# Performance work log

Measured on AMD Instinct MI355X. Metric: run time of the kernel, lower is better.

The kernel has to match this reference:

```python
import jax, jax.numpy as jnp
import numpy as np

NEG_INF = -1e30

def masked_softmax(logits, mask, axis):
    # mask broadcastable to logits; 1 = keep, 0 = mask out
    masked = jnp.where(mask > 0, logits, NEG_INF)
    return jax.nn.softmax(masked, axis=axis)

def setup_inputs() -> dict:
    key = jax.random.key(0)
    ks = jax.random.split(key, 6)
    B, H, C, Q = 64, 128, 1024, 128
    c = jax.random.normal(ks[0], (B, H, C), dtype=jnp.float32)
    q = jax.random.normal(ks[1], (B, H, Q), dtype=jnp.float32)
    c_mask = jnp.ones((B, C), dtype=jnp.float32)
    q_mask = jnp.ones((B, Q), dtype=jnp.float32)
    # xavier_uniform for (H,1): bound = sqrt(6/(H+1))
    bnd_v = float(np.sqrt(6.0 / (H + 1)))
    context_weights = jax.random.uniform(ks[2], (H, 1), minval=-bnd_v, maxval=bnd_v, dtype=jnp.float32)
    query_weights = jax.random.uniform(ks[3], (H, 1), minval=-bnd_v, maxval=bnd_v, dtype=jnp.float32)
    # xavier_uniform for (1,1,H): fan_in=1, fan_out=H -> bound = sqrt(6/(1+H))
    cq_weights = jax.random.uniform(ks[4], (1, 1, H), minval=-bnd_v, maxval=bnd_v, dtype=jnp.float32)
    bias = jnp.zeros((1,), dtype=jnp.float32)
    return {"c": c, "q": q, "c_mask": c_mask, "q_mask": q_mask,
            "context_weights": context_weights, "query_weights": query_weights,
            "cq_weights": cq_weights, "bias": bias}

def reference(c, q, c_mask, q_mask, context_weights, query_weights, cq_weights, bias):
    # to (B, len, H)
    c = jnp.swapaxes(c, 1, 2)  # (B, c_len, H)
    q = jnp.swapaxes(q, 1, 2)  # (B, q_len, H)
    B, c_len, H = c.shape
    q_len = q.shape[1]
    # trilinear similarity: (B, c_len, q_len)
    s0 = c @ context_weights                         # (B, c_len, 1)
    s1 = jnp.swapaxes(q @ query_weights, 1, 2)       # (B, 1, q_len)
    s2 = jnp.einsum('bch,bqh->bcq', c * cq_weights, q)
    S = s0 + s1 + s2 + bias
    a_att = masked_softmax(S, q_mask[:, None, :], axis=2)  # softmax over q_len
    b_att = masked_softmax(S, c_mask[:, :, None], axis=1)  # softmax over c_len
    a = jnp.einsum('bcq,bqh->bch', a_att, q)
    b = jnp.einsum('bcq,bkq,bkh->bch', a_att, b_att, c)
    x = jnp.concatenate([c, a, c * a, c * b], axis=2)  # (B, c_len, 4H)
    return jnp.swapaxes(x, 1, 2)  # (B, 4H, c_len)
```

## Files before the change

kernel.cpp:

```cpp
#include <hip/hip_runtime.h>
#include <math.h>

#define NEG_HUGE -1e30f
constexpr int B_ = 64, H_ = 128, C_ = 1024, Q_ = 128;

typedef __bf16 bf16x8 __attribute__((ext_vector_type(8)));
typedef float f32x4 __attribute__((ext_vector_type(4)));
typedef short short8 __attribute__((ext_vector_type(8)));
typedef short short4s __attribute__((ext_vector_type(4)));

__device__ __forceinline__ float bs2f(short s) {
  unsigned u = ((unsigned)(unsigned short)s) << 16;
  float f; __builtin_memcpy(&f, &u, 4); return f;
}
__device__ __forceinline__ short f2bs(float f) {
  unsigned u; __builtin_memcpy(&u, &f, 4);
  u = (u + 0x7fffu + ((u >> 16) & 1u)) >> 16;
  return (short)u;
}

__global__ __launch_bounds__(256) void kTc(const float* __restrict__ cin,
                                           const float* __restrict__ ctxw,
                                           short* __restrict__ cT,
                                           float* __restrict__ s0p) {
  __shared__ float T[64 * 69];
  const int t = threadIdx.x;
  const int c0 = blockIdx.x * 64, h0 = blockIdx.y * 64, b = blockIdx.z;
  {
    const int row = t >> 2, off = t & 3;
    const float* src = cin + (b * H_ + h0 + row) * C_ + c0;
#pragma unroll
    for (int j = 0; j < 4; ++j) {
      float4 v = *(const float4*)&src[off * 16 + j * 4];
      int cbase = off * 16 + j * 4;
      T[row * 69 + cbase + 0] = v.x;
      T[row * 69 + cbase + 1] = v.y;
      T[row * 69 + cbase + 2] = v.z;
      T[row * 69 + cbase + 3] = v.w;
    }
  }
  __syncthreads();
  {
    const int c = t >> 2, offh = t & 3;
    short* dst = cT + (b * C_ + c0 + c) * H_ + h0;
#pragma unroll
    for (int j = 0; j < 4; ++j) {
      int hs = offh * 16 + j * 4;
      short4s v;
      v[0] = f2bs(T[(hs + 0) * 69 + c]);
      v[1] = f2bs(T[(hs + 1) * 69 + c]);
      v[2] = f2bs(T[(hs + 2) * 69 + c]);
      v[3] = f2bs(T[(hs + 3) * 69 + c]);
      *(short4s*)&dst[hs] = v;
    }
  }
  if (t < 64) {
    float acc = 0.f;
#pragma unroll 8
    for (int h = 0; h < 64; ++h) acc += T[h * 69 + t] * ctxw[h0 + h];
    s0p[blockIdx.y * (B_ * C_) + b * C_ + c0 + t] = acc;
  }
}

__global__ __launch_bounds__(256) void kq(const float* __restrict__ qin,
                                          const float* __restrict__ qw,
                                          const float* __restrict__ cqw,
                                          const float* __restrict__ qmask,
                                          short* __restrict__ qTw,
                                          short* __restrict__ qbf,
                                          float* __restrict__ s1m) {
  __shared__ float T[64 * 130];
  const int t = threadIdx.x;
  const int q0 = blockIdx.x * 64, b = blockIdx.y;
#pragma unroll
  for (int p = 0; p < 8; ++p) {
    int fidx = t + 256 * p;
    int h = fidx >> 4, seg = fidx & 15;
    float4 v = *(const float4*)&qin[(b * H_ + h) * Q_ + q0 + seg * 4];
    T[(seg * 4 + 0) * 130 + h] = v.x;
    T[(seg * 4 + 1) * 130 + h] = v.y;
    T[(seg * 4 + 2) * 130 + h] = v.z;
    T[(seg * 4 + 3) * 130 + h] = v.w;
    short4s o; o[0] = f2bs(v.x); o[1] = f2bs(v.y); o[2] = f2bs(v.z); o[3] = f2bs(v.w);
    *(short4s*)&qbf[(b * H_ + h) * Q_ + q0 + seg * 4] = o;
  }
  __syncthreads();
  if (t < 64) {
    float acc = 0.f;
#pragma unroll 8
    for (int h = 0; h < 128; ++h) acc += T[t * 130 + h] * qw[h];
    float qm = (qmask[b * Q_ + q0 + t] > 0.f) ? 0.f : NEG_HUGE;
    s1m[b * Q_ + q0 + t] = acc + qm;
  }
  {
    const int q = t >> 2, off = t & 3;
    short* dst = qTw + (b * Q_ + q0 + q) * H_;
#pragma unroll
    for (int j = 0; j < 4; ++j) {
      int hbv = off * 32 + j * 8;
      short8 v;
#pragma unroll
      for (int i = 0; i < 8; ++i) v[i] = f2bs(T[q * 130 + hbv + i] * cqw[hbv + i]);
      *(short8*)&dst[hbv] = v;
    }
  }
}

__global__ __launch_bounds__(256) void k1_mfma(
    const short* __restrict__ cT, const short* __restrict__ qTw,
    const float* __restrict__ s1m, const float* __restrict__ cmask,
    const float* __restrict__ s0p,
    short* __restrict__ a_att, short* __restrict__ ePT,
    float* __restrict__ pcm, float* __restrict__ pcs) {
  __shared__ __align__(16) char uni[34816];
  __shared__ float s1mL[128], scolL[128], pw[512], mpL[128];
  short* AL = (short*)uni;
  short* BL = (short*)(uni + 10240);
  short* RP = (short*)uni;

  const int t = threadIdx.x;
  const int w = t >> 6, l = t & 63, quad = l >> 4, lcol = l & 15;
  const int bx = blockIdx.x, b = blockIdx.y, c0 = bx * 128;

  if (t < 128) {
    s1mL[t] = s1m[b * Q_ + t];
    float cm = (cmask[b * C_ + c0 + t] > 0.f) ? 0.f : NEG_HUGE;
    scolL[t] = cm + s0p[b * C_ + c0 + t] + s0p[B_ * C_ + b * C_ + c0 + t];
  }

  f32x4 acc[2][8];
#pragma unroll
  for (int mt = 0; mt < 2; ++mt)
#pragma unroll
    for (int nt = 0; nt < 8; ++nt) acc[mt][nt] = (f32x4){0.f, 0.f, 0.f, 0.f};

  const int ar = t >> 2, aoff = t & 3;

  for (int kc = 0; kc < 4; ++kc) {
    const int h0 = kc * 32;
    *(short8*)&AL[ar * 40 + aoff * 8] =
        *(const short8*)&cT[(b * C_ + c0 + ar) * H_ + h0 + aoff * 8];
    *(short8*)&AL[(64 + ar) * 40 + aoff * 8] =
        *(const short8*)&cT[(b * C_ + c0 + 64 + ar) * H_ + h0 + aoff * 8];
    *(short8*)&BL[ar * 40 + aoff * 8] =
        *(const short8*)&qTw[(b * Q_ + ar) * H_ + h0 + aoff * 8];
    *(short8*)&BL[(64 + ar) * 40 + aoff * 8] =
        *(const short8*)&qTw[(b * Q_ + 64 + ar) * H_ + h0 + aoff * 8];
    __syncthreads();
    bf16x8 af0 = *(bf16x8*)&AL[(w * 32 + lcol) * 40 + quad * 8];
    bf16x8 af1 = *(bf16x8*)&AL[(w * 32 + 16 + lcol) * 40 + quad * 8];
#pragma unroll
    for (int nt = 0; nt < 8; ++nt) {
      bf16x8 bfrag = *(bf16x8*)&BL[(nt * 16 + lcol) * 40 + quad * 8];
      acc[0][nt] = __builtin_amdgcn_mfma_f32_16x16x32_bf16(af0, bfrag, acc[0][nt], 0, 0, 0);
      acc[1][nt] = __builtin_amdgcn_mfma_f32_16x16x32_bf16(af1, bfrag, acc[1][nt], 0, 0, 0);
    }
    __syncthreads();
  }

  float s1v[8];
#pragma unroll
  for (int nt = 0; nt < 8; ++nt) s1v[nt] = s1mL[nt * 16 + lcol];
  float rm[2][4], inv[2][4];
#pragma unroll
  for (int mt = 0; mt < 2; ++mt)
#pragma unroll
    for (int r = 0; r < 4; ++r) {
      float m = -INFINITY;
#pragma unroll
      for (int nt = 0; nt < 8; ++nt) m = fmaxf(m, acc[mt][nt][r] + s1v[nt]);
      rm[mt][r] = m;
    }
#pragma unroll
  for (int d = 1; d <= 8; d <<= 1)
#pragma unroll
    for (int mt = 0; mt < 2; ++mt)
#pragma unroll
      for (int r = 0; r < 4; ++r)
        rm[mt][r] = fmaxf(rm[mt][r], __shfl_xor(rm[mt][r], d));
#pragma unroll
  for (int mt = 0; mt < 2; ++mt)
#pragma unroll
    for (int r = 0; r < 4; ++r) {
      float s = 0.f;
#pragma unroll
      for (int nt = 0; nt < 8; ++nt)
        s += __expf(acc[mt][nt][r] + s1v[nt] - rm[mt][r]);
      inv[mt][r] = s;
    }
#pragma unroll
  for (int d = 1; d <= 8; d <<= 1)
#pragma unroll
    for (int mt = 0; mt < 2; ++mt)
#pragma unroll
      for (int r = 0; r < 4; ++r)
        inv[mt][r] += __shfl_xor(inv[mt][r], d);
#pragma unroll
  for (int mt = 0; mt < 2; ++mt)
#pragma unroll
    for (int r = 0; r < 4; ++r) inv[mt][r] = 1.f / inv[mt][r];

#pragma unroll
  for (int mt = 0; mt < 2; ++mt)
#pragma unroll
    for (int nt = 0; nt < 8; ++nt)
#pragma unroll
      for (int r = 0; r < 4; ++r) {
        int row = w * 32 + mt * 16 + quad * 4 + r;
        int col = nt * 16 + lcol;
        float v = __expf(acc[mt][nt][r] + s1v[nt] - rm[mt][r]) * inv[mt][r];
        RP[row * 136 + col] = f2bs(v);
      }
  __syncthreads();
  {
    const int row = t >> 1, half = t & 1;
    short* dst = a_att + (b * C_ + c0 + row) * Q_ + half * 64;
    const short* srcp = RP + row * 136 + half * 64;
#pragma unroll
    for (int j = 0; j < 8; ++j) *(short8*)&dst[j * 8] = *(const short8*)&srcp[j * 8];
  }

  float cs0[2][4];
#pragma unroll
  for (int mt = 0; mt < 2; ++mt)
#pragma unroll
    for (int r = 0; r < 4; ++r)
      cs0[mt][r] = scolL[w * 32 + mt * 16 + quad * 4 + r];
  float pmv[8];
#pragma unroll
  for (int nt = 0; nt < 8; ++nt) {
    float m = -INFINITY;
#pragma unroll
    for (int mt = 0; mt < 2; ++mt)
#pragma unroll
      for (int r = 0; r < 4; ++r) m = fmaxf(m, acc[mt][nt][r] + cs0[mt][r]);
    pmv[nt] = m;
  }
#pragma unroll
  for (int nt = 0; nt < 8; ++nt) {
    pmv[nt] = fmaxf(pmv[nt], __shfl_xor(pmv[nt], 16));
    pmv[nt] = fmaxf(pmv[nt], __shfl_xor(pmv[nt], 32));
  }
  if (l < 16) {
#pragma unroll
    for (int nt = 0; nt < 8; ++nt) pw[w * 128 + nt * 16 + lcol] = pmv[nt];
  }
  __syncthreads();
  if (t < 128) {
    float m = fmaxf(fmaxf(pw[t], pw[128 + t]), fmaxf(pw[256 + t], pw[384 + t]));
    mpL[t] = m;
    pcm[(b * 8 + bx) * Q_ + t] = m;
  }
  __syncthreads();
  float mpv[8];
#pragma unroll
  for (int nt = 0; nt < 8; ++nt) mpv[nt] = mpL[nt * 16 + lcol];
  float psv[8];
#pragma unroll
  for (int nt = 0; nt < 8; ++nt) {
    float s = 0.f;
#pragma unroll
    for (int mt = 0; mt < 2; ++mt)
#pragma unroll
      for (int r = 0; r < 4; ++r)
        s += __expf(acc[mt][nt][r] + cs0[mt][r] - mpv[nt]);
    psv[nt] = s;
  }
#pragma unroll
  for (int nt = 0; nt < 8; ++nt) {
    psv[nt] += __shfl_xor(psv[nt], 16);
    psv[nt] += __shfl_xor(psv[nt], 32);
  }
  if (l < 16) {
#pragma unroll
    for (int nt = 0; nt < 8; ++nt) pw[w * 128 + nt * 16 + lcol] = psv[nt];
  }
  __syncthreads();
  if (t < 128) pcs[(b * 8 + bx) * Q_ + t] = pw[t] + pw[128 + t] + pw[256 + t] + pw[384 + t];

#pragma unroll
  for (int mt = 0; mt < 2; ++mt)
#pragma unroll
    for (int nt = 0; nt < 8; ++nt)
#pragma unroll
      for (int r = 0; r < 4; ++r) {
        int qq = nt * 16 + lcol;
        int cl = w * 32 + mt * 16 + quad * 4 + r;
        float v = __expf(acc[mt][nt][r] + cs0[mt][r] - mpv[nt]);
        RP[qq * 136 + cl] = f2bs(v);
      }
  __syncthreads();
  {
    const int qq = t >> 1, half = t & 1;
    short* dst = ePT + (b * Q_ + qq) * C_ + c0 + half * 64;
    const short* srcp = RP + qq * 136 + half * 64;
#pragma unroll
    for (int j = 0; j < 8; ++j) *(short8*)&dst[j * 8] = *(const short8*)&srcp[j * 8];
  }
}

__global__ __launch_bounds__(128) void k2b(const float* __restrict__ pcm,
                                           const float* __restrict__ pcs,
                                           float* __restrict__ scale_t,
                                           float* __restrict__ inv_cs) {
  const int b = blockIdx.x, q = threadIdx.x;
  float m[8]; float M = -INFINITY;
#pragma unroll
  for (int k = 0; k < 8; ++k) { m[k] = pcm[(b * 8 + k) * Q_ + q]; M = fmaxf(M, m[k]); }
  float s = 0.f;
#pragma unroll
  for (int k = 0; k < 8; ++k) {
    float sc = __expf(m[k] - M);
    scale_t[(b * 8 + k) * Q_ + q] = sc;
    s += pcs[(b * 8 + k) * Q_ + q] * sc;
  }
  inv_cs[b * Q_ + q] = 1.f / s;
}

__global__ __launch_bounds__(256) void krs(short* __restrict__ ePT,
                                           const float* __restrict__ scale_t) {
  const int gid = blockIdx.x * 256 + threadIdx.x;
  const int e = gid * 8;
  const int c = e & 1023, q = (e >> 10) & 127, b = e >> 17;
  const float s = scale_t[(b * 8 + (c >> 7)) * Q_ + q];
  short8 v = *(short8*)&ePT[e];
  short8 o;
#pragma unroll
  for (int i = 0; i < 8; ++i) o[i] = f2bs(bs2f(v[i]) * s);
  *(short8*)&ePT[e] = o;
}

__global__ __launch_bounds__(256) void k3_T(
    const short* __restrict__ ePs, const float* __restrict__ cin,
    float* __restrict__ Tpart) {
  __shared__ __align__(16) char uni[34816];
  short* AL = (short*)uni;
  short* BL = (short*)(uni + 10240);
  float* RPF = (float*)uni;
  const int t = threadIdx.x;
  const int w = t >> 6, l = t & 63, quad = l >> 4, lcol = l & 15;
  const int hb = blockIdx.x * 64, kc = blockIdx.y, b = blockIdx.z;

  f32x4 acc[2][4];
#pragma unroll
  for (int mt = 0; mt < 2; ++mt)
#pragma unroll
    for (int nt = 0; nt < 4; ++nt) acc[mt][nt] = (f32x4){0.f, 0.f, 0.f, 0.f};

  const int ar = t >> 2, aoff = t & 3;
  for (int ck = 0; ck < 8; ++ck) {
    const int coff = kc * 256 + ck * 32;
    *(short8*)&AL[ar * 40 + aoff * 8] =
        *(const short8*)&ePs[(b * Q_ + ar) * C_ + coff + aoff * 8];
    *(short8*)&AL[(64 + ar) * 40 + aoff * 8] =
        *(const short8*)&ePs[(b * Q_ + 64 + ar) * C_ + coff + aoff * 8];
    {
      const float* srcp = cin + (b * H_ + hb + ar) * C_ + coff + aoff * 8;
      short8 o;
#pragma unroll
      for (int i = 0; i < 8; ++i) o[i] = f2bs(srcp[i]);
      *(short8*)&BL[ar * 40 + aoff * 8] = o;
    }
    __syncthreads();
    bf16x8 af0 = *(bf16x8*)&AL[(w * 32 + lcol) * 40 + quad * 8];
    bf16x8 af1 = *(bf16x8*)&AL[(w * 32 + 16 + lcol) * 40 + quad * 8];
#pragma unroll
    for (int nt = 0; nt < 4; ++nt) {
      bf16x8 bfrag = *(bf16x8*)&BL[(nt * 16 + lcol) * 40 + quad * 8];
      acc[0][nt] = __builtin_amdgcn_mfma_f32_16x16x32_bf16(af0, bfrag, acc[0][nt], 0, 0, 0);
      acc[1][nt] = __builtin_amdgcn_mfma_f32_16x16x32_bf16(af1, bfrag, acc[1][nt], 0, 0, 0);
    }
    __syncthreads();
  }
#pragma unroll
  for (int mt = 0; mt < 2; ++mt)
#pragma unroll
    for (int nt = 0; nt < 4; ++nt)
#pragma unroll
      for (int r = 0; r < 4; ++r)
        RPF[(nt * 16 + lcol) * 136 + (w * 32 + mt * 16 + quad * 4 + r)] = acc[mt][nt][r];
  __syncthreads();
  {
    float* Tp = Tpart + (size_t)kc * (B_ * H_ * Q_) + ((size_t)b * H_ + hb) * Q_;
    const int lr = t >> 5, coln = (t & 31) * 4;
#pragma unroll
    for (int iter = 0; iter < 8; ++iter) {
      int hl = iter * 8 + lr;
      *(float4*)&Tp[hl * Q_ + coln] = *(float4*)&RPF[hl * 136 + coln];
    }
  }
}

__global__ __launch_bounds__(256) void k3b(const float* __restrict__ Tpart,
                                           const float* __restrict__ inv_cs,
                                           short* __restrict__ TmT) {
  const int gid = blockIdx.x * 256 + threadIdx.x;
  const int e = gid * 4;
  const int q0 = e & 127, b = e >> 14;
  float4 s = make_float4(0.f, 0.f, 0.f, 0.f);
#pragma unroll
  for (int k = 0; k < 4; ++k) {
    float4 v = *(const float4*)&Tpart[(size_t)k * (B_ * H_ * Q_) + e];
    s.x += v.x; s.y += v.y; s.z += v.z; s.w += v.w;
  }
  float4 ic = *(const float4*)&inv_cs[b * Q_ + q0];
  short4s o;
  o[0] = f2bs(s.x * ic.x); o[1] = f2bs(s.y * ic.y);
  o[2] = f2bs(s.z * ic.z); o[3] = f2bs(s.w * ic.w);
  *(short4s*)&TmT[e] = o;
}

__global__ __launch_bounds__(256) void k4_out(
    const short* __restrict__ a_att, const short* __restrict__ qbf,
    const short* __restrict__ TmT, const float* __restrict__ cin,
    float* __restrict__ out) {
  __shared__ __align__(16) char uni[34816];
  short* AL = (short*)uni;
  short* B1 = (short*)(uni + 10240);
  short* B2 = (short*)(uni + 15360);
  float* RPF = (float*)uni;
  const int t = threadIdx.x;
  const int w = t >> 6, l = t & 63, quad = l >> 4, lcol = l & 15;
  const int c0 = blockIdx.x * 128, hb = blockIdx.y * 64, b = blockIdx.z;

  f32x4 accA[2][4], accB[2][4];
#pragma unroll
  for (int mt = 0; mt < 2; ++mt)
#pragma unroll
    for (int nt = 0; nt < 4; ++nt) {
      accA[mt][nt] = (f32x4){0.f, 0.f, 0.f, 0.f};
      accB[mt][nt] = (f32x4){0.f, 0.f, 0.f, 0.f};
    }

  const int ar = t >> 2, aoff = t & 3;
  for (int kc = 0; kc < 4; ++kc) {
    const int q0 = kc * 32;
    *(short8*)&AL[ar * 40 + aoff * 8] =
        *(const short8*)&a_att[(b * C_ + c0 + ar) * Q_ + q0 + aoff * 8];
    *(short8*)&AL[(64 + ar) * 40 + aoff * 8] =
        *(const short8*)&a_att[(b * C_ + c0 + 64 + ar) * Q_ + q0 + aoff * 8];
    *(short8*)&B1[ar * 40 + aoff * 8] =
        *(const short8*)&qbf[(b * H_ + hb + ar) * Q_ + q0 + aoff * 8];
    *(short8*)&B2[ar * 40 + aoff * 8] =
        *(const short8*)&TmT[(b * H_ + hb + ar) * Q_ + q0 + aoff * 8];
    __syncthreads();
    bf16x8 af0 = *(bf16x8*)&AL[(w * 32 + lcol) * 40 + quad * 8];
    bf16x8 af1 = *(bf16x8*)&AL[(w * 32 + 16 + lcol) * 40 + quad * 8];
#pragma unroll
    for (int nt = 0; nt < 4; ++nt) {
      bf16x8 bq = *(bf16x8*)&B1[(nt * 16 + lcol) * 40 + quad * 8];
      bf16x8 bt = *(bf16x8*)&B2[(nt * 16 + lcol) * 40 + quad * 8];
      accA[0][nt] = __builtin_amdgcn_mfma_f32_16x16x32_bf16(af0, bq, accA[0][nt], 0, 0, 0);
      accA[1][nt] = __builtin_amdgcn_mfma_f32_16x16x32_bf16(af1, bq, accA[1][nt], 0, 0, 0);
      accB[0][nt] = __builtin_amdgcn_mfma_f32_16x16x32_bf16(af0, bt, accB[0][nt], 0, 0, 0);
      accB[1][nt] = __builtin_amdgcn_mfma_f32_16x16x32_bf16(af1, bt, accB[1][nt], 0, 0, 0);
    }
    __syncthreads();
  }

  const int lr = t >> 5, coln = (t & 31) * 4;
  float* ob = out + (size_t)b * 512 * 1024;
  float4 cvv[8];

#pragma unroll
  for (int mt = 0; mt < 2; ++mt)
#pragma unroll
    for (int nt = 0; nt < 4; ++nt)
#pragma unroll
      for (int r = 0; r < 4; ++r)
        RPF[(nt * 16 + lcol) * 136 + (w * 32 + mt * 16 + quad * 4 + r)] = accA[mt][nt][r];
  __syncthreads();
#pragma unroll
  for (int iter = 0; iter < 8; ++iter) {
    int hl = iter * 8 + lr;
    int hrow = hb + hl;
    float4 la = *(float4*)&RPF[hl * 136 + coln];
    float4 cv = *(const float4*)&cin[(b * H_ + hrow) * C_ + c0 + coln];
    cvv[iter] = cv;
    *(float4*)&ob[(size_t)hrow * 1024 + c0 + coln] = cv;
    *(float4*)&ob[(size_t)(128 + hrow) * 1024 + c0 + coln] = la;
    float4 p = make_float4(cv.x * la.x, cv.y * la.y, cv.z * la.z, cv.w * la.w);
    *(float4*)&ob[(size_t)(256 + hrow) * 1024 + c0 + coln] = p;
  }
  __syncthreads();
#pragma unroll
  for (int mt = 0; mt < 2; ++mt)
#pragma unroll
    for (int nt = 0; nt < 4; ++nt)
#pragma unroll
      for (int r = 0; r < 4; ++r)
        RPF[(nt * 16 + lcol) * 136 + (w * 32 + mt * 16 + quad * 4 + r)] = accB[mt][nt][r];
  __syncthreads();
#pragma unroll
  for (int iter = 0; iter < 8; ++iter) {
    int hl = iter * 8 + lr;
    int hrow = hb + hl;
    float4 lb = *(float4*)&RPF[hl * 136 + coln];
    float4 cv = cvv[iter];
    float4 p = make_float4(cv.x * lb.x, cv.y * lb.y, cv.z * lb.z, cv.w * lb.w);
    *(float4*)&ob[(size_t)(384 + hrow) * 1024 + c0 + coln] = p;
  }
}

extern "C" void kernel_launch(void* const* d_in, const int* in_sizes, int n_in,
                              void* d_out, int out_size, void* d_ws, size_t ws_size,
                              hipStream_t stream) {
  const float* c     = (const float*)d_in[0];
  const float* q     = (const float*)d_in[1];
  const float* cmask = (const float*)d_in[2];
  const float* qmask = (const float*)d_in[3];
  const float* ctxw  = (const float*)d_in[4];
  const float* qw    = (const float*)d_in[5];
  const float* cqw   = (const float*)d_in[6];
  float* out = (float*)d_out;

  char* ws = (char*)d_ws;
  short* cT     = (short*)(ws);
  float* Tpart  = (float*)(ws);
  short* qTw    = (short*)(ws + 16777216);
  short* TmT    = (short*)(ws + 16777216);
  short* qbf    = (short*)(ws + 18874368);
  short* a_att  = (short*)(ws + 20971520);
  short* ePT    = (short*)(ws + 37748736);
  float* s0p    = (float*)(ws + 54525952);
  float* s1m    = (float*)(ws + 55050240);
  float* pcm    = (float*)(ws + 55083008);
  float* pcs    = (float*)(ws + 55345152);
  float* scalet = (float*)(ws + 55607296);
  float* inv_cs = (float*)(ws + 55869440);

  kTc<<<dim3(16, 2, B_), dim3(256), 0, stream>>>(c, ctxw, cT, s0p);
  kq<<<dim3(2, B_), dim3(256), 0, stream>>>(q, qw, cqw, qmask, qTw, qbf, s1m);
  k1_mfma<<<dim3(8, B_), dim3(256), 0, stream>>>(cT, qTw, s1m, cmask, s0p,
                                                 a_att, ePT, pcm, pcs);
  k2b<<<dim3(B_), dim3(128), 0, stream>>>(pcm, pcs, scalet, inv_cs);
  krs<<<dim3(4096), dim3(256), 0, stream>>>(ePT, scalet);
  k3_T<<<dim3(2, 4, B_), dim3(256), 0, stream>>>(ePT, c, Tpart);
  k3b<<<dim3(1024), dim3(256), 0, stream>>>(Tpart, inv_cs, TmT);
  k4_out<<<dim3(8, 2, B_), dim3(256), 0, stream>>>(a_att, qbf, TmT, c, out);
}
```

Baseline: 263.1 us.

## Fold column-softmax rescale into k3_T, reuse exps, use nontemporal output stores

Removes the k2b and krs kernels. The per-block column-max rescale and inverse sum are now computed at the start of k3_T and applied while ePT tiles are loaded, so the extra read-modify-write pass over the ePT buffer disappears. In k1_mfma the row-softmax exponentials are kept in registers, and the column-softmax numerators are derived from them with one exp per row/column factor instead of a fresh exp per element. The final stores in k4_out become nontemporal. The risks are redundant per-block recomputation of the rescale factors and slightly different rounding from the factored exponent, which could overflow for extreme logit ranges.

After: 238.7 us. -9.3%, faster.

```diff
diff --git a/kernel.cpp b/kernel.cpp
--- a/kernel.cpp
+++ b/kernel.cpp
@@ -17,6 +17,10 @@
   unsigned u; __builtin_memcpy(&u, &f, 4);
   u = (u + 0x7fffu + ((u >> 16) & 1u)) >> 16;
   return (short)u;
+}
+__device__ __forceinline__ void nts4(float* p, float4 v) {
+  f32x4 x; x[0] = v.x; x[1] = v.y; x[2] = v.z; x[3] = v.w;
+  __builtin_nontemporal_store(x, (f32x4*)p);
 }
 
 __global__ __launch_bounds__(256) void kTc(const float* __restrict__ cin,
@@ -161,7 +165,14 @@
   float s1v[8];
 #pragma unroll
   for (int nt = 0; nt < 8; ++nt) s1v[nt] = s1mL[nt * 16 + lcol];
-  float rm[2][4], inv[2][4];
+  float cs0[2][4];
+#pragma unroll
+  for (int mt = 0; mt < 2; ++mt)
+#pragma unroll
+    for (int r = 0; r < 4; ++r)
+      cs0[mt][r] = scolL[w * 32 + mt * 16 + quad * 4 + r];
+
+  float rm[2][4];
 #pragma unroll
   for (int mt = 0; mt < 2; ++mt)
 #pragma unroll
@@ -178,14 +189,43 @@
 #pragma unroll
       for (int r = 0; r < 4; ++r)
         rm[mt][r] = fmaxf(rm[mt][r], __shfl_xor(rm[mt][r], d));
+
+  float pmv[8];
+#pragma unroll
+  for (int nt = 0; nt < 8; ++nt) {
+    float m = -INFINITY;
+#pragma unroll
+    for (int mt = 0; mt < 2; ++mt)
+#pragma unroll
+      for (int r = 0; r < 4; ++r) m = fmaxf(m, acc[mt][nt][r] + cs0[mt][r]);
+    pmv[nt] = m;
+  }
+#pragma unroll
+  for (int nt = 0; nt < 8; ++nt) {
+    pmv[nt] = fmaxf(pmv[nt], __shfl_xor(pmv[nt], 16));
+    pmv[nt] = fmaxf(pmv[nt], __shfl_xor(pmv[nt], 32));
+  }
+  if (l < 16) {
+#pragma unroll
+    for (int nt = 0; nt < 8; ++nt) pw[w * 128 + nt * 16 + lcol] = pmv[nt];
+  }
+
+#pragma unroll
+  for (int mt = 0; mt < 2; ++mt)
+#pragma unroll
+    for (int nt = 0; nt < 8; ++nt)
+#pragma unroll
+      for (int r = 0; r < 4; ++r)
+        acc[mt][nt][r] = __expf(acc[mt][nt][r] + s1v[nt] - rm[mt][r]);
+
+  float inv[2][4];
 #pragma unroll
   for (int mt = 0; mt < 2; ++mt)
 #pragma unroll
     for (int r = 0; r < 4; ++r) {
       float s = 0.f;
 #pragma unroll
-      for (int nt = 0; nt < 8; ++nt)
-        s += __expf(acc[mt][nt][r] + s1v[nt] - rm[mt][r]);
+      for (int nt = 0; nt < 8; ++nt) s += acc[mt][nt][r];
       inv[mt][r] = s;
     }
 #pragma unroll
@@ -208,8 +248,7 @@
       for (int r = 0; r < 4; ++r) {
         int row = w * 32 + mt * 16 + quad * 4 + r;
         int col = nt * 16 + lcol;
-        float v = __expf(acc[mt][nt][r] + s1v[nt] - rm[mt][r]) * inv[mt][r];
-        RP[row * 136 + col] = f2bs(v);
+        RP[row * 136 + col] = f2bs(acc[mt][nt][r] * inv[mt][r]);
       }
   __syncthreads();
   {
@@ -219,32 +258,6 @@
 #pragma unroll
     for (int j = 0; j < 8; ++j) *(short8*)&dst[j * 8] = *(const short8*)&srcp[j * 8];
   }
-
-  float cs0[2][4];
-#pragma unroll
-  for (int mt = 0; mt < 2; ++mt)
-#pragma unroll
-    for (int r = 0; r < 4; ++r)
-      cs0[mt][r] = scolL[w * 32 + mt * 16 + quad * 4 + r];
-  float pmv[8];
-#pragma unroll
-  for (int nt = 0; nt < 8; ++nt) {
-    float m = -INFINITY;
-#pragma unroll
-    for (int mt = 0; mt < 2; ++mt)
-#pragma unroll
-      for (int r = 0; r < 4; ++r) m = fmaxf(m, acc[mt][nt][r] + cs0[mt][r]);
-    pmv[nt] = m;
-  }
-#pragma unroll
-  for (int nt = 0; nt < 8; ++nt) {
-    pmv[nt] = fmaxf(pmv[nt], __shfl_xor(pmv[nt], 16));
-    pmv[nt] = fmaxf(pmv[nt], __shfl_xor(pmv[nt], 32));
-  }
-  if (l < 16) {
-#pragma unroll
-    for (int nt = 0; nt < 8; ++nt) pw[w * 128 + nt * 16 + lcol] = pmv[nt];
-  }
   __syncthreads();
   if (t < 128) {
     float m = fmaxf(fmaxf(pw[t], pw[128 + t]), fmaxf(pw[256 + t], pw[384 + t]));
@@ -255,15 +268,26 @@
   float mpv[8];
 #pragma unroll
   for (int nt = 0; nt < 8; ++nt) mpv[nt] = mpL[nt * 16 + lcol];
+
+  float crm[2][4];
+#pragma unroll
+  for (int mt = 0; mt < 2; ++mt)
+#pragma unroll
+    for (int r = 0; r < 4; ++r) crm[mt][r] = cs0[mt][r] + rm[mt][r];
   float psv[8];
 #pragma unroll
   for (int nt = 0; nt < 8; ++nt) {
+    const float sm = s1v[nt] + mpv[nt];
+    const int qq = nt * 16 + lcol;
     float s = 0.f;
 #pragma unroll
     for (int mt = 0; mt < 2; ++mt)
 #pragma unroll
-      for (int r = 0; r < 4; ++r)
-        s += __expf(acc[mt][nt][r] + cs0[mt][r] - mpv[nt]);
+      for (int r = 0; r < 4; ++r) {
+        float v = acc[mt][nt][r] * __expf(crm[mt][r] - sm);
+        s += v;
+        RP[qq * 136 + (w * 32 + mt * 16 + quad * 4 + r)] = f2bs(v);
+      }
     psv[nt] = s;
   }
 #pragma unroll
@@ -277,19 +301,6 @@
   }
   __syncthreads();
   if (t < 128) pcs[(b * 8 + bx) * Q_ + t] = pw[t] + pw[128 + t] + pw[256 + t] + pw[384 + t];
-
-#pragma unroll
-  for (int mt = 0; mt < 2; ++mt)
-#pragma unroll
-    for (int nt = 0; nt < 8; ++nt)
-#pragma unroll
-      for (int r = 0; r < 4; ++r) {
-        int qq = nt * 16 + lcol;
-        int cl = w * 32 + mt * 16 + quad * 4 + r;
-        float v = __expf(acc[mt][nt][r] + cs0[mt][r] - mpv[nt]);
-        RP[qq * 136 + cl] = f2bs(v);
-      }
-  __syncthreads();
   {
     const int qq = t >> 1, half = t & 1;
     short* dst = ePT + (b * Q_ + qq) * C_ + c0 + half * 64;
@@ -299,48 +310,32 @@
   }
 }
 
-__global__ __launch_bounds__(128) void k2b(const float* __restrict__ pcm,
-                                           const float* __restrict__ pcs,
-                                           float* __restrict__ scale_t,
-                                           float* __restrict__ inv_cs) {
-  const int b = blockIdx.x, q = threadIdx.x;
-  float m[8]; float M = -INFINITY;
-#pragma unroll
-  for (int k = 0; k < 8; ++k) { m[k] = pcm[(b * 8 + k) * Q_ + q]; M = fmaxf(M, m[k]); }
-  float s = 0.f;
-#pragma unroll
-  for (int k = 0; k < 8; ++k) {
-    float sc = __expf(m[k] - M);
-    scale_t[(b * 8 + k) * Q_ + q] = sc;
-    s += pcs[(b * 8 + k) * Q_ + q] * sc;
-  }
-  inv_cs[b * Q_ + q] = 1.f / s;
-}
-
-__global__ __launch_bounds__(256) void krs(short* __restrict__ ePT,
-                                           const float* __restrict__ scale_t) {
-  const int gid = blockIdx.x * 256 + threadIdx.x;
-  const int e = gid * 8;
-  const int c = e & 1023, q = (e >> 10) & 127, b = e >> 17;
-  const float s = scale_t[(b * 8 + (c >> 7)) * Q_ + q];
-  short8 v = *(short8*)&ePT[e];
-  short8 o;
-#pragma unroll
-  for (int i = 0; i < 8; ++i) o[i] = f2bs(bs2f(v[i]) * s);
-  *(short8*)&ePT[e] = o;
-}
-
 __global__ __launch_bounds__(256) void k3_T(
-    const short* __restrict__ ePs, const float* __restrict__ cin,
+    const short* __restrict__ ePT, const float* __restrict__ cin,
+    const float* __restrict__ pcm, const float* __restrict__ pcs,
     float* __restrict__ Tpart) {
   __shared__ __align__(16) char uni[34816];
   short* AL = (short*)uni;
   short* BL = (short*)(uni + 10240);
   float* RPF = (float*)uni;
+  __shared__ float scA[2][128];
+  __shared__ float icL[128];
   const int t = threadIdx.x;
   const int w = t >> 6, l = t & 63, quad = l >> 4, lcol = l & 15;
   const int hb = blockIdx.x * 64, kc = blockIdx.y, b = blockIdx.z;
 
+  if (t < 128) {
+    float m[8]; float M = -INFINITY;
+#pragma unroll
+    for (int k = 0; k < 8; ++k) { m[k] = pcm[(b * 8 + k) * Q_ + t]; M = fmaxf(M, m[k]); }
+    float s = 0.f;
+#pragma unroll
+    for (int k = 0; k < 8; ++k) s += pcs[(b * 8 + k) * Q_ + t] * __expf(m[k] - M);
+    icL[t] = 1.f / s;
+    scA[0][t] = __expf(m[kc * 2 + 0] - M);
+    scA[1][t] = __expf(m[kc * 2 + 1] - M);
+  }
+
   f32x4 acc[2][4];
 #pragma unroll
   for (int mt = 0; mt < 2; ++mt)
@@ -348,12 +343,26 @@
     for (int nt = 0; nt < 4; ++nt) acc[mt][nt] = (f32x4){0.f, 0.f, 0.f, 0.f};
 
   const int ar = t >> 2, aoff = t & 3;
+  __syncthreads();
+  const float s00 = scA[0][ar], s01 = scA[0][64 + ar];
+  const float s10 = scA[1][ar], s11 = scA[1][64 + ar];
+
   for (int ck = 0; ck < 8; ++ck) {
     const int coff = kc * 256 + ck * 32;
-    *(short8*)&AL[ar * 40 + aoff * 8] =
-        *(const short8*)&ePs[(b * Q_ + ar) * C_ + coff + aoff * 8];
-    *(short8*)&AL[(64 + ar) * 40 + aoff * 8] =
-        *(const short8*)&ePs[(b * Q_ + 64 + ar) * C_ + coff + aoff * 8];
+    const float sA0 = (ck < 4) ? s00 : s10;
+    const float sA1 = (ck < 4) ? s01 : s11;
+    {
+      short8 v0 = *(const short8*)&ePT[(b * Q_ + ar) * C_ + coff + aoff * 8];
+      short8 v1 = *(const short8*)&ePT[(b * Q_ + 64 + ar) * C_ + coff + aoff * 8];
+      short8 o0, o1;
+#pragma unroll
+      for (int i = 0; i < 8; ++i) {
+        o0[i] = f2bs(bs2f(v0[i]) * sA0);
+        o1[i] = f2bs(bs2f(v1[i]) * sA1);
+      }
+      *(short8*)&AL[ar * 40 + aoff * 8] = o0;
+      *(short8*)&AL[(64 + ar) * 40 + aoff * 8] = o1;
+    }
     {
       const float* srcp = cin + (b * H_ + hb + ar) * C_ + coff + aoff * 8;
       short8 o;
@@ -383,30 +392,29 @@
   {
     float* Tp = Tpart + (size_t)kc * (B_ * H_ * Q_) + ((size_t)b * H_ + hb) * Q_;
     const int lr = t >> 5, coln = (t & 31) * 4;
+    float4 ic = *(const float4*)&icL[coln];
 #pragma unroll
     for (int iter = 0; iter < 8; ++iter) {
       int hl = iter * 8 + lr;
-      *(float4*)&Tp[hl * Q_ + coln] = *(float4*)&RPF[hl * 136 + coln];
+      float4 v = *(float4*)&RPF[hl * 136 + coln];
+      v.x *= ic.x; v.y *= ic.y; v.z *= ic.z; v.w *= ic.w;
+      *(float4*)&Tp[hl * Q_ + coln] = v;
     }
   }
 }
 
 __global__ __launch_bounds__(256) void k3b(const float* __restrict__ Tpart,
-                                           const float* __restrict__ inv_cs,
                                            short* __restrict__ TmT) {
   const int gid = blockIdx.x * 256 + threadIdx.x;
   const int e = gid * 4;
-  const int q0 = e & 127, b = e >> 14;
   float4 s = make_float4(0.f, 0.f, 0.f, 0.f);
 #pragma unroll
   for (int k = 0; k < 4; ++k) {
     float4 v = *(const float4*)&Tpart[(size_t)k * (B_ * H_ * Q_) + e];
     s.x += v.x; s.y += v.y; s.z += v.z; s.w += v.w;
   }
-  float4 ic = *(const float4*)&inv_cs[b * Q_ + q0];
   short4s o;
-  o[0] = f2bs(s.x * ic.x); o[1] = f2bs(s.y * ic.y);
-  o[2] = f2bs(s.z * ic.z); o[3] = f2bs(s.w * ic.w);
+  o[0] = f2bs(s.x); o[1] = f2bs(s.y); o[2] = f2bs(s.z); o[3] = f2bs(s.w);
   *(short4s*)&TmT[e] = o;
 }
 
@@ -477,10 +485,10 @@
     float4 la = *(float4*)&RPF[hl * 136 + coln];
     float4 cv = *(const float4*)&cin[(b * H_ + hrow) * C_ + c0 + coln];
     cvv[iter] = cv;
-    *(float4*)&ob[(size_t)hrow * 1024 + c0 + coln] = cv;
-    *(float4*)&ob[(size_t)(128 + hrow) * 1024 + c0 + coln] = la;
+    nts4(&ob[(size_t)hrow * 1024 + c0 + coln], cv);
+    nts4(&ob[(size_t)(128 + hrow) * 1024 + c0 + coln], la);
     float4 p = make_float4(cv.x * la.x, cv.y * la.y, cv.z * la.z, cv.w * la.w);
-    *(float4*)&ob[(size_t)(256 + hrow) * 1024 + c0 + coln] = p;
+    nts4(&ob[(size_t)(256 + hrow) * 1024 + c0 + coln], p);
   }
   __syncthreads();
 #pragma unroll
@@ -498,7 +506,7 @@
     float4 lb = *(float4*)&RPF[hl * 136 + coln];
     float4 cv = cvv[iter];
     float4 p = make_float4(cv.x * lb.x, cv.y * lb.y, cv.z * lb.z, cv.w * lb.w);
-    *(float4*)&ob[(size_t)(384 + hrow) * 1024 + c0 + coln] = p;
+    nts4(&ob[(size_t)(384 + hrow) * 1024 + c0 + coln], p);
   }
 }
 
@@ -526,16 +534,12 @@
   float* s1m    = (float*)(ws + 55050240);
   float* pcm    = (float*)(ws + 55083008);
   float* pcs    = (float*)(ws + 55345152);
-  float* scalet = (float*)(ws + 55607296);
-  float* inv_cs = (float*)(ws + 55869440);
 
   kTc<<<dim3(16, 2, B_), dim3(256), 0, stream>>>(c, ctxw, cT, s0p);
   kq<<<dim3(2, B_), dim3(256), 0, stream>>>(q, qw, cqw, qmask, qTw, qbf, s1m);
   k1_mfma<<<dim3(8, B_), dim3(256), 0, stream>>>(cT, qTw, s1m, cmask, s0p,
                                                  a_att, ePT, pcm, pcs);
-  k2b<<<dim3(B_), dim3(128), 0, stream>>>(pcm, pcs, scalet, inv_cs);
-  krs<<<dim3(4096), dim3(256), 0, stream>>>(ePT, scalet);
-  k3_T<<<dim3(2, 4, B_), dim3(256), 0, stream>>>(ePT, c, Tpart);
-  k3b<<<dim3(1024), dim3(256), 0, stream>>>(Tpart, inv_cs, TmT);
+  k3_T<<<dim3(2, 4, B_), dim3(256), 0, stream>>>(ePT, c, pcm, pcs, Tpart);
+  k3b<<<dim3(1024), dim3(256), 0, stream>>>(Tpart, TmT);
   k4_out<<<dim3(8, 2, B_), dim3(256), 0, stream>>>(a_att, qbf, TmT, c, out);
 }
```
